# Performance work log

Measured on AMD Instinct MI355X. Metric: run time of the kernel, lower is better.

## Reference

```python
import jax, jax.numpy as jnp
import numpy as np

L, B, E, H = 4096, 4, 1024, 16
HD = E // H
EPS = 1e-4


def setup_inputs() -> dict:
    key = jax.random.key(0)
    ks = jax.random.split(key, 9)
    s = 1.0 / np.sqrt(E)
    return {
        "query": jax.random.normal(ks[0], (L, B, E), jnp.float32),
        "key_": jax.random.normal(ks[1], (L, B, E), jnp.float32),
        "value": jax.random.normal(ks[2], (L, B, E), jnp.float32),
        "Wq": jax.random.normal(ks[3], (E, E), jnp.float32) * s,
        "bq": jnp.zeros((E,), jnp.float32),
        "Wk": jax.random.normal(ks[4], (E, E), jnp.float32) * s,
        "bk": jnp.zeros((E,), jnp.float32),
        "Wv": jax.random.normal(ks[5], (E, E), jnp.float32) * s,
        "bv": jnp.zeros((E,), jnp.float32),
    }


def _heads(x):
    # (L, B, E) -> (B*H, L, HD)
    l = x.shape[0]
    return x.reshape(l, B * H, HD).transpose(1, 0, 2)


def reference(query, key_, value, Wq, bq, Wk, bk, Wv, bv):
    tgt_len = query.shape[0]
    src_len = key_.shape[0]
    q = _heads(query @ Wq.T + bq)
    k = _heads(key_ @ Wk.T + bk)
    v = _heads(value @ Wv.T + bv)
    # relu feature map (use_relu=True, constant=0)
    q = jax.nn.relu(q)
    k = jax.nn.relu(k)
    m = max(src_len, tgt_len)
    # pi/2 * arange(1, m+1) / m
    ang = (jnp.pi / 2) * jnp.arange(1, m + 1, dtype=q.dtype) / m  # (m,)
    sin = jnp.sin(ang)[None, :, None]
    cos = jnp.cos(ang)[None, :, None]
    q_ = jnp.concatenate([q * sin[:, :tgt_len], q * cos[:, :tgt_len]], axis=-1)  # (n, L, 2HD)
    k_ = jnp.concatenate([k * sin[:, :src_len], k * cos[:, :src_len]], axis=-1)
    # non-causal linear attention
    kv_ = jnp.einsum('nld,nlm->ndm', k_, v)                       # (n, 2HD, HD)
    z_ = 1.0 / jnp.maximum(jnp.einsum('nld,nd->nl', q_, k_.sum(axis=1)), EPS)
    attn = jnp.einsum('nld,ndm,nl->nlm', q_, kv_, z_)             # (n, L, HD)
    out = attn.transpose(1, 0, 2).reshape(tgt_len, B, E)
    return out
```

## Files before the change

kernel.cpp:

```cpp
#include <hip/hip_runtime.h>
#include <hip/hip_bf16.h>


typedef unsigned short ushortt;
typedef unsigned int u32;
typedef __attribute__((ext_vector_type(8))) short bf16x8;
typedef __attribute__((ext_vector_type(4))) float f32x4;

#define L_DIM 4096
#define B_DIM 4
#define E_DIM 1024

#define KV_CH 8
#define KV_LCH (L_DIM / KV_CH)
#define KV_LT 32

__device__ __forceinline__ ushortt f2bf(float f) {
    union { float f; u32 u; } v; v.f = f;
    u32 u = v.u;
    u += 0x7FFFu + ((u >> 16) & 1u);
    return (ushortt)(u >> 16);
}
__device__ __forceinline__ float bf2f(ushortt h) {
    union { u32 u; float f; } v; v.u = ((u32)h) << 16;
    return v.f;
}

__device__ __forceinline__ void gl_lds16(const void* g, void* l) {
    __builtin_amdgcn_global_load_lds(
        (const __attribute__((address_space(1))) unsigned int*)g,
        (__attribute__((address_space(3))) unsigned int*)l, 16, 0, 0);
}

__global__ __launch_bounds__(256) void k_cvtW(
    const float* __restrict__ W, ushortt* __restrict__ Wb)
{
    const int i = (blockIdx.x * 256 + threadIdx.x) * 4;
    const float4 v = *reinterpret_cast<const float4*>(W + i);
    ushortt o[4] = { f2bf(v.x), f2bf(v.y), f2bf(v.z), f2bf(v.w) };
    *reinterpret_cast<uint2*>(Wb + i) = *reinterpret_cast<uint2*>(o);
}

__global__ __launch_bounds__(256) void k_cvtX(
    const float* __restrict__ X, ushortt* __restrict__ Xb)
{
    const int i = (blockIdx.x * 256 + threadIdx.x) * 4;
    const float4 v = *reinterpret_cast<const float4*>(X + i);
    ushortt o[4] = { f2bf(v.x), f2bf(v.y), f2bf(v.z), f2bf(v.w) };
    *reinterpret_cast<uint2*>(Xb + i) = *reinterpret_cast<uint2*>(o);
}

__global__ __launch_bounds__(256) void k_gemmB(
    const ushortt* __restrict__ Xb, const ushortt* __restrict__ Wb,
    const float* __restrict__ bias,
    float* __restrict__ Of, ushortt* __restrict__ Ob, const int p)
{
    __shared__ char sA[8192];
    __shared__ char sB[8192];

    const int t = threadIdx.x;
    const int ln = t & 63;
    const int wv = t >> 6;
    const int wr = wv >> 1, wc = wv & 1;

    const int orig = blockIdx.x;
    const int bid = (orig & 7) * 128 + (orig >> 3);
    const int mblk = (bid >> 3) * 128;
    const int nblk = (bid & 7) * 128;

    f32x4 acc[4][4];
#pragma unroll
    for (int i = 0; i < 4; i++)
#pragma unroll
        for (int j = 0; j < 4; j++) acc[i][j] = (f32x4){0.f, 0.f, 0.f, 0.f};

    const int rowIn = ln >> 2;
    const int srcE  = ((ln & 3) ^ ((ln >> 3) & 3)) << 3;

    const int g   = ln >> 4;
    const int r15 = ln & 15;
    const int sw  = ((r15 >> 1) & 3) << 4;

    for (int k0 = 0; k0 < 1024; k0 += 32) {
        __syncthreads();
#pragma unroll
        for (int c = 0; c < 2; c++) {
            const int ch = wv * 2 + c;
            const int row = ch * 16 + rowIn;
            gl_lds16(Xb + (size_t)(mblk + row) * E_DIM + k0 + srcE, sA + ch * 1024);
            gl_lds16(Wb + (size_t)(nblk + row) * E_DIM + k0 + srcE, sB + ch * 1024);
        }
        __syncthreads();

        bf16x8 va[4], vb[4];
#pragma unroll
        for (int i = 0; i < 4; i++) {
            const int row = wr * 64 + i * 16 + r15;
            va[i] = *reinterpret_cast<const bf16x8*>(sA + row * 64 + ((g * 16) ^ sw));
        }
#pragma unroll
        for (int j = 0; j < 4; j++) {
            const int n = wc * 64 + j * 16 + r15;
            vb[j] = *reinterpret_cast<const bf16x8*>(sB + n * 64 + ((g * 16) ^ sw));
        }
#pragma unroll
        for (int i = 0; i < 4; i++)
#pragma unroll
            for (int j = 0; j < 4; j++)
                acc[i][j] = __builtin_amdgcn_mfma_f32_16x16x32_bf16(va[i], vb[j], acc[i][j], 0, 0, 0);
    }

#pragma unroll
    for (int j = 0; j < 4; j++) {
        const int col = nblk + wc * 64 + j * 16 + r15;
        const float bj = bias[col];
#pragma unroll
        for (int i = 0; i < 4; i++) {
            const int row0 = mblk + wr * 64 + i * 16 + g * 4;
#pragma unroll
            for (int r = 0; r < 4; r++) {
                float v = acc[i][j][r] + bj;
                if (p < 2) v = fmaxf(v, 0.0f);
                if (p == 0) Of[(size_t)(row0 + r) * E_DIM + col] = v;
                else        Ob[(size_t)(row0 + r) * E_DIM + col] = f2bf(v);
            }
        }
    }
}

__global__ __launch_bounds__(256) void k_kv3(
    const ushortt* __restrict__ Kb, const ushortt* __restrict__ Vb,
    float* __restrict__ pm, float* __restrict__ pd)
{
    __shared__ float sk[KV_LT][128];
    __shared__ float sv[KV_LT][64];

    const int head = blockIdx.x;
    const int b = head >> 4, hh = head & 15;
    const int t = threadIdx.x;
    const int mq = t & 7;
    const int dq = t >> 3;
    const int l0base = blockIdx.y * KV_LCH;

    float acc[4][8];
    float ksum[4];
#pragma unroll
    for (int i = 0; i < 4; i++) {
        ksum[i] = 0.0f;
#pragma unroll
        for (int j = 0; j < 8; j++) acc[i][j] = 0.0f;
    }

    const size_t headoff = (size_t)hh * 64;

    for (int l0 = l0base; l0 < l0base + KV_LCH; l0 += KV_LT) {
        __syncthreads();
#pragma unroll
        for (int i = 0; i < 2; i++) {
            const int j = t + 256 * i;
            const int l = j >> 4;
            const int c4 = (j & 15) << 2;
            const size_t rowb = ((size_t)(l0 + l) * B_DIM + b) * E_DIM + headoff;
            const uint2 kraw = *reinterpret_cast<const uint2*>(Kb + rowb + c4);
            const uint2 vraw = *reinterpret_cast<const uint2*>(Vb + rowb + c4);
            const float ang = 1.5707963267948966f * (float)(l0 + l + 1) * (1.0f / 4096.0f);
            const float sn = sinf(ang), cs = cosf(ang);
            const float k0 = bf2f((ushortt)(kraw.x & 0xffffu));
            const float k1 = bf2f((ushortt)(kraw.x >> 16));
            const float k2 = bf2f((ushortt)(kraw.y & 0xffffu));
            const float k3 = bf2f((ushortt)(kraw.y >> 16));
            *reinterpret_cast<float4*>(&sk[l][c4]) =
                make_float4(sn * k0, sn * k1, sn * k2, sn * k3);
            *reinterpret_cast<float4*>(&sk[l][64 + c4]) =
                make_float4(cs * k0, cs * k1, cs * k2, cs * k3);
            *reinterpret_cast<float4*>(&sv[l][c4]) =
                make_float4(bf2f((ushortt)(vraw.x & 0xffffu)),
                            bf2f((ushortt)(vraw.x >> 16)),
                            bf2f((ushortt)(vraw.y & 0xffffu)),
                            bf2f((ushortt)(vraw.y >> 16)));
        }
        __syncthreads();
#pragma unroll 8
        for (int l = 0; l < KV_LT; l++) {
            const float4 a4 = *reinterpret_cast<const float4*>(&sk[l][dq << 2]);
            const float4 v0 = *reinterpret_cast<const float4*>(&sv[l][mq << 3]);
            const float4 v1 = *reinterpret_cast<const float4*>(&sv[l][(mq << 3) + 4]);
            const float av[4] = { a4.x, a4.y, a4.z, a4.w };
            const float vv[8] = { v0.x, v0.y, v0.z, v0.w, v1.x, v1.y, v1.z, v1.w };
#pragma unroll
            for (int i = 0; i < 4; i++) {
#pragma unroll
                for (int j = 0; j < 8; j++) acc[i][j] += av[i] * vv[j];
                ksum[i] += av[i];
            }
        }
    }

    float* dstm = pm + ((size_t)blockIdx.y * 64 + head) * 8192;
    float* dstd = pd + ((size_t)blockIdx.y * 64 + head) * 128;
    const int d0 = dq << 2, m0 = mq << 3;
#pragma unroll
    for (int i = 0; i < 4; i++) {
        *reinterpret_cast<float4*>(&dstm[(d0 + i) * 64 + m0]) =
            make_float4(acc[i][0], acc[i][1], acc[i][2], acc[i][3]);
        *reinterpret_cast<float4*>(&dstm[(d0 + i) * 64 + m0 + 4]) =
            make_float4(acc[i][4], acc[i][5], acc[i][6], acc[i][7]);
        if (mq == 0) dstd[d0 + i] = ksum[i];
    }
}

__global__ __launch_bounds__(256) void k_kvred(
    const float* __restrict__ pm, const float* __restrict__ pd,
    float* __restrict__ kvm, float* __restrict__ kvd)
{
    const int bid = blockIdx.x, t = threadIdx.x;
    if (bid < 512) {
        const int g = bid * 256 + t;
        const int head = g >> 11, r = g & 2047;
        float4 s = make_float4(0.f, 0.f, 0.f, 0.f);
#pragma unroll
        for (int c = 0; c < KV_CH; c++) {
            const float4 v = reinterpret_cast<const float4*>(pm)[((size_t)(c * 64 + head) << 11) + r];
            s.x += v.x; s.y += v.y; s.z += v.z; s.w += v.w;
        }
        reinterpret_cast<float4*>(kvm)[g] = s;
    } else {
#pragma unroll
        for (int it = 0; it < 8; it++) {
            const int idx = it * 256 + t;
            const int head = idx >> 5, r = idx & 31;
            float4 s = make_float4(0.f, 0.f, 0.f, 0.f);
#pragma unroll
            for (int c = 0; c < KV_CH; c++) {
                const float4 v = reinterpret_cast<const float4*>(pd)[((size_t)(c * 64 + head) << 5) + r];
                s.x += v.x; s.y += v.y; s.z += v.z; s.w += v.w;
            }
            reinterpret_cast<float4*>(kvd)[idx] = s;
        }
    }
}

__global__ __launch_bounds__(256) void k_attn2(
    float* qout, const float* __restrict__ kvm, const float* __restrict__ kvd)
{
    __shared__ float skv[128][64];
    __shared__ float skd[128];
    __shared__ float sq[32][132];

    const int t = threadIdx.x;
    const int head = blockIdx.x;
    const int b = head >> 4, hh = head & 15;
    const int l0 = blockIdx.y * 32;

    const float* kvh = kvm + (size_t)head * (128 * 64);

#pragma unroll
    for (int c = 0; c < 8; c++) {
        const int idx = t + 256 * c;
        const int d = idx >> 4, m4 = (idx & 15) << 2;
        *reinterpret_cast<float4*>(&skv[d][m4]) =
            *reinterpret_cast<const float4*>(kvh + d * 64 + m4);
    }
    if (t < 128) skd[t] = kvd[(size_t)head * 128 + t];

    const size_t qbase = ((size_t)l0 * B_DIM + b) * E_DIM + (size_t)hh * 64;
#pragma unroll
    for (int c = 0; c < 2; c++) {
        const int idx = t + 256 * c;
        const int l = idx >> 4, q4 = (idx & 15) << 2;
        const float4 v = *reinterpret_cast<const float4*>(
            qout + qbase + (size_t)l * (B_DIM * E_DIM) + q4);
        const float ang = 1.5707963267948966f * (float)(l0 + l + 1) * (1.0f / 4096.0f);
        const float sn = sinf(ang), cs = cosf(ang);
        *reinterpret_cast<float4*>(&sq[l][q4]) =
            make_float4(sn * v.x, sn * v.y, sn * v.z, sn * v.w);
        *reinterpret_cast<float4*>(&sq[l][64 + q4]) =
            make_float4(cs * v.x, cs * v.y, cs * v.z, cs * v.w);
    }
    __syncthreads();

    const int tx = t & 15, ty = t >> 4;
    const int r = ty * 2, m0 = tx * 4;

    float4 acc[2] = { make_float4(0.f, 0.f, 0.f, 0.f), make_float4(0.f, 0.f, 0.f, 0.f) };
    float accd[2] = { 0.f, 0.f };

#pragma unroll 4
    for (int d0 = 0; d0 < 128; d0 += 4) {
        const float4 kd4 = *reinterpret_cast<const float4*>(&skd[d0]);
        float4 qv[2];
#pragma unroll
        for (int i = 0; i < 2; i++)
            qv[i] = *reinterpret_cast<const float4*>(&sq[r + i][d0]);
#pragma unroll
        for (int dd = 0; dd < 4; dd++) {
            const float4 kvv = *reinterpret_cast<const float4*>(&skv[d0 + dd][m0]);
            const float kdv = (dd == 0) ? kd4.x : (dd == 1) ? kd4.y : (dd == 2) ? kd4.z : kd4.w;
#pragma unroll
            for (int i = 0; i < 2; i++) {
                const float qs = (dd == 0) ? qv[i].x : (dd == 1) ? qv[i].y
                               : (dd == 2) ? qv[i].z : qv[i].w;
                acc[i].x += qs * kvv.x;
                acc[i].y += qs * kvv.y;
                acc[i].z += qs * kvv.z;
                acc[i].w += qs * kvv.w;
                accd[i] += qs * kdv;
            }
        }
    }

#pragma unroll
    for (int i = 0; i < 2; i++) {
        const float z = 1.0f / fmaxf(accd[i], 1e-4f);
        float4 vo = make_float4(acc[i].x * z, acc[i].y * z, acc[i].z * z, acc[i].w * z);
        *reinterpret_cast<float4*>(
            qout + qbase + (size_t)(r + i) * (B_DIM * E_DIM) + m0) = vo;
    }
}

extern "C" void kernel_launch(void* const* d_in, const int* in_sizes, int n_in,
                              void* d_out, int out_size, void* d_ws, size_t ws_size,
                              hipStream_t stream) {
    (void)in_sizes; (void)n_in; (void)out_size; (void)ws_size;
    const float* xq = (const float*)d_in[0];
    const float* xk = (const float*)d_in[1];
    const float* xv = (const float*)d_in[2];
    const float* wq = (const float*)d_in[3];
    const float* bq = (const float*)d_in[4];
    const float* wk = (const float*)d_in[5];
    const float* bk = (const float*)d_in[6];
    const float* wv = (const float*)d_in[7];
    const float* bv = (const float*)d_in[8];
    float* out = (float*)d_out;

    char* ws = (char*)d_ws;
    ushortt* Kb  = (ushortt*)(ws);
    ushortt* Vb  = (ushortt*)(ws + 33554432);
    ushortt* Wb  = (ushortt*)(ws + 67108864);
    float*   kvm = (float*)(ws + 67108864);
    float*   kvd = (float*)(ws + 67108864 + 2097152);
    ushortt* Xqb = (ushortt*)(ws);
    ushortt* Wqb = (ushortt*)(ws + 33554432);

    ushortt* Xkb = (ushortt*)d_out;
    ushortt* Xvb = (ushortt*)((char*)d_out + 33554432);
    float*   pm  = (float*)d_out;
    float*   pd  = (float*)((char*)d_out + 16777216);

    dim3 blk(256);
    k_cvtW<<<dim3(1024), blk, 0, stream>>>(wk, Wb);
    k_cvtX<<<dim3(16384), blk, 0, stream>>>(xk, Xkb);
    k_gemmB<<<dim3(1024), blk, 0, stream>>>(Xkb, Wb, bk, (float*)nullptr, Kb, 1);
    k_cvtW<<<dim3(1024), blk, 0, stream>>>(wv, Wb);
    k_cvtX<<<dim3(16384), blk, 0, stream>>>(xv, Xvb);
    k_gemmB<<<dim3(1024), blk, 0, stream>>>(Xvb, Wb, bv, (float*)nullptr, Vb, 2);
    k_kv3<<<dim3(64, KV_CH), blk, 0, stream>>>(Kb, Vb, pm, pd);
    k_kvred<<<dim3(513), blk, 0, stream>>>(pm, pd, kvm, kvd);
    k_cvtW<<<dim3(1024), blk, 0, stream>>>(wq, Wqb);
    k_cvtX<<<dim3(16384), blk, 0, stream>>>(xq, Xqb);
    k_gemmB<<<dim3(1024), blk, 0, stream>>>(Xqb, Wqb, bq, out, (ushortt*)nullptr, 0);
    k_attn2<<<dim3(64, 128), blk, 0, stream>>>(out, kvm, kvd);
}
```

Measured before the change: 564.1 us.

## Double-buffer GEMM LDS staging and enlarge attention row tile to 64

The projection GEMM now keeps two LDS buffers and issues the global-to-LDS loads for the next K slice before computing on the current one. This halves the barriers per iteration and overlaps load latency with MFMA work. Separately, the attention kernel handles 64 query rows per block with 4 rows per thread, so the KV tile loaded into LDS is reused across more rows. The cost is doubled LDS in the GEMM and more LDS and registers in the attention kernel, which may lower occupancy.

```diff
diff --git a/kernel.cpp b/kernel.cpp
--- a/kernel.cpp
+++ b/kernel.cpp
@@ -55,8 +55,8 @@
     const float* __restrict__ bias,
     float* __restrict__ Of, ushortt* __restrict__ Ob, const int p)
 {
-    __shared__ char sA[8192];
-    __shared__ char sB[8192];
+    __shared__ char sA[2][8192];
+    __shared__ char sB[2][8192];
 
     const int t = threadIdx.x;
     const int ln = t & 63;
@@ -81,33 +81,42 @@
     const int r15 = ln & 15;
     const int sw  = ((r15 >> 1) & 3) << 4;
 
-    for (int k0 = 0; k0 < 1024; k0 += 32) {
-        __syncthreads();
+    auto stage = [&](int buf, int k0) {
 #pragma unroll
         for (int c = 0; c < 2; c++) {
             const int ch = wv * 2 + c;
             const int row = ch * 16 + rowIn;
-            gl_lds16(Xb + (size_t)(mblk + row) * E_DIM + k0 + srcE, sA + ch * 1024);
-            gl_lds16(Wb + (size_t)(nblk + row) * E_DIM + k0 + srcE, sB + ch * 1024);
-        }
-        __syncthreads();
+            gl_lds16(Xb + (size_t)(mblk + row) * E_DIM + k0 + srcE, &sA[buf][ch * 1024]);
+            gl_lds16(Wb + (size_t)(nblk + row) * E_DIM + k0 + srcE, &sB[buf][ch * 1024]);
+        }
+    };
+
+    stage(0, 0);
+    __syncthreads();
+
+    int cur = 0;
+    for (int k0 = 0; k0 < 1024; k0 += 32) {
+        if (k0 + 32 < 1024) stage(cur ^ 1, k0 + 32);
 
         bf16x8 va[4], vb[4];
 #pragma unroll
         for (int i = 0; i < 4; i++) {
             const int row = wr * 64 + i * 16 + r15;
-            va[i] = *reinterpret_cast<const bf16x8*>(sA + row * 64 + ((g * 16) ^ sw));
+            va[i] = *reinterpret_cast<const bf16x8*>(&sA[cur][row * 64 + ((g * 16) ^ sw)]);
         }
 #pragma unroll
         for (int j = 0; j < 4; j++) {
             const int n = wc * 64 + j * 16 + r15;
-            vb[j] = *reinterpret_cast<const bf16x8*>(sB + n * 64 + ((g * 16) ^ sw));
+            vb[j] = *reinterpret_cast<const bf16x8*>(&sB[cur][n * 64 + ((g * 16) ^ sw)]);
         }
 #pragma unroll
         for (int i = 0; i < 4; i++)
 #pragma unroll
             for (int j = 0; j < 4; j++)
                 acc[i][j] = __builtin_amdgcn_mfma_f32_16x16x32_bf16(va[i], vb[j], acc[i][j], 0, 0, 0);
+
+        __syncthreads();
+        cur ^= 1;
     }
 
 #pragma unroll
@@ -240,17 +249,17 @@
     }
 }
 
-__global__ __launch_bounds__(256) void k_attn2(
+__global__ __launch_bounds__(256) void k_attn3(
     float* qout, const float* __restrict__ kvm, const float* __restrict__ kvd)
 {
     __shared__ float skv[128][64];
     __shared__ float skd[128];
-    __shared__ float sq[32][132];
+    __shared__ float sq[64][132];
 
     const int t = threadIdx.x;
     const int head = blockIdx.x;
     const int b = head >> 4, hh = head & 15;
-    const int l0 = blockIdx.y * 32;
+    const int l0 = blockIdx.y * 64;
 
     const float* kvh = kvm + (size_t)head * (128 * 64);
 
@@ -265,7 +274,7 @@
 
     const size_t qbase = ((size_t)l0 * B_DIM + b) * E_DIM + (size_t)hh * 64;
 #pragma unroll
-    for (int c = 0; c < 2; c++) {
+    for (int c = 0; c < 4; c++) {
         const int idx = t + 256 * c;
         const int l = idx >> 4, q4 = (idx & 15) << 2;
         const float4 v = *reinterpret_cast<const float4*>(
@@ -280,24 +289,29 @@
     __syncthreads();
 
     const int tx = t & 15, ty = t >> 4;
-    const int r = ty * 2, m0 = tx * 4;
-
-    float4 acc[2] = { make_float4(0.f, 0.f, 0.f, 0.f), make_float4(0.f, 0.f, 0.f, 0.f) };
-    float accd[2] = { 0.f, 0.f };
+    const int r = ty * 4, m0 = tx * 4;
+
+    float4 acc[4];
+    float accd[4];
+#pragma unroll
+    for (int i = 0; i < 4; i++) {
+        acc[i] = make_float4(0.f, 0.f, 0.f, 0.f);
+        accd[i] = 0.f;
+    }
 
 #pragma unroll 4
     for (int d0 = 0; d0 < 128; d0 += 4) {
         const float4 kd4 = *reinterpret_cast<const float4*>(&skd[d0]);
-        float4 qv[2];
-#pragma unroll
-        for (int i = 0; i < 2; i++)
+        float4 qv[4];
+#pragma unroll
+        for (int i = 0; i < 4; i++)
             qv[i] = *reinterpret_cast<const float4*>(&sq[r + i][d0]);
 #pragma unroll
         for (int dd = 0; dd < 4; dd++) {
             const float4 kvv = *reinterpret_cast<const float4*>(&skv[d0 + dd][m0]);
             const float kdv = (dd == 0) ? kd4.x : (dd == 1) ? kd4.y : (dd == 2) ? kd4.z : kd4.w;
 #pragma unroll
-            for (int i = 0; i < 2; i++) {
+            for (int i = 0; i < 4; i++) {
                 const float qs = (dd == 0) ? qv[i].x : (dd == 1) ? qv[i].y
                                : (dd == 2) ? qv[i].z : qv[i].w;
                 acc[i].x += qs * kvv.x;
@@ -310,7 +324,7 @@
     }
 
 #pragma unroll
-    for (int i = 0; i < 2; i++) {
+    for (int i = 0; i < 4; i++) {
         const float z = 1.0f / fmaxf(accd[i], 1e-4f);
         float4 vo = make_float4(acc[i].x * z, acc[i].y * z, acc[i].z * z, acc[i].w * z);
         *reinterpret_cast<float4*>(
@@ -359,5 +373,5 @@
     k_cvtW<<<dim3(1024), blk, 0, stream>>>(wq, Wqb);
     k_cvtX<<<dim3(16384), blk, 0, stream>>>(xq, Xqb);
     k_gemmB<<<dim3(1024), blk, 0, stream>>>(Xqb, Wqb, bq, out, (ushortt*)nullptr, 0);
-    k_attn2<<<dim3(64, 128), blk, 0, stream>>>(out, kvm, kvd);
-}
+    k_attn3<<<dim3(64, 64), blk, 0, stream>>>(out, kvm, kvd);
+}
```

After: 565.8 us. Within noise of the previous version (+0.3%).
